# Kernel tuning notes

Hardware: AMD Instinct MI355X
Metric: run time of the kernel (lower is better)

Reference implementation:

```python
import jax, jax.numpy as jnp
import numpy as np
from jax import lax

B, H, W_IN, C = 32, 32, 32, 128   # NHWC input
KH, KW = 3, 3                     # kernel size (padding 'same', stride 1)
F = 512                           # filters


def setup_inputs() -> dict:
    key = jax.random.key(0)
    ks = jax.random.split(key, 10)
    # sparse factor shapes: (KH*KW*C, 1152), (1152, F), (F, F)
    d0, d1, d2, d3 = KH * KW * C, 1152, F, F
    x = jax.random.normal(ks[0], (B, H, W_IN, C), dtype=jnp.float32)
    k0 = jax.random.normal(ks[1], (d0, d1), dtype=jnp.float32) * (1.0 / np.sqrt(d0))
    k1 = jax.random.normal(ks[2], (d1, d2), dtype=jnp.float32) * (1.0 / np.sqrt(d1))
    k2 = jax.random.normal(ks[3], (d2, d3), dtype=jnp.float32) * (1.0 / np.sqrt(d2))
    # fixed binary sparsity masks (K.constant in the original build)
    m0 = jax.random.bernoulli(ks[4], 0.1, (d0, d1)).astype(jnp.float32)
    m1 = jax.random.bernoulli(ks[5], 0.1, (d1, d2)).astype(jnp.float32)
    m2 = jax.random.bernoulli(ks[6], 0.1, (d2, d3)).astype(jnp.float32)
    scale = jax.random.normal(ks[7], (1,), dtype=jnp.float32)
    bias = jax.random.normal(ks[8], (F,), dtype=jnp.float32) * 0.01
    return {"x": x, "k0": k0, "k1": k1, "k2": k2,
            "m0": m0, "m1": m1, "m2": m2, "scale": scale, "bias": bias}


def reference(x, k0, k1, k2, m0, m1, m2, scale, bias):
    # Chained masked sparse factors collapse (associativity) to one effective
    # filter matrix of shape (KH*KW*C, F); the im2col row flatten order in the
    # original is (h, w, c), which matches an HWIO reshape exactly.
    w_eff = (k0 * m0) @ (k1 * m1) @ (k2 * m2)          # (KH*KW*C, F)
    w = (w_eff * scale[0]).reshape(KH, KW, C, F)        # fold scalar scale into kernel
    out = lax.conv_general_dilated(
        x, w, window_strides=(1, 1), padding='SAME',
        dimension_numbers=('NHWC', 'HWIO', 'NHWC'))     # (B, H, W, F)
    return out + bias
```

## Files before the change

### kernel.cpp

```cpp
#include <hip/hip_runtime.h>

typedef __attribute__((ext_vector_type(8))) short short8;
typedef __attribute__((ext_vector_type(4))) float f32x4;

typedef __attribute__((address_space(1))) const unsigned gas_u32;
typedef __attribute__((address_space(3))) unsigned las_u32;

static __device__ __forceinline__ void g2l16(const void* g, void* l) {
  __builtin_amdgcn_global_load_lds((gas_u32*)g, (las_u32*)l, 16, 0, 0);
}

static __device__ __forceinline__ short f2bf(float f) {
  union { float f; unsigned u; } v; v.f = f;
  unsigned r = (v.u + 0x7FFFu + ((v.u >> 16) & 1u)) >> 16;
  return (short)r;
}

__global__ __launch_bounds__(256) void k_prep(const float* __restrict__ x,
                                              const float* __restrict__ k0f,
                                              const float* __restrict__ m0f,
                                              const float* __restrict__ scf,
                                              const float* __restrict__ k1f,
                                              const float* __restrict__ m1f,
                                              const float* __restrict__ k2f,
                                              const float* __restrict__ m2f,
                                              short* __restrict__ xbp,
                                              short* __restrict__ w1b,
                                              short* __restrict__ w2T,
                                              short* __restrict__ w3T) {
  __shared__ float tile[32][33];
  const int bb = blockIdx.x, tid = threadIdx.x;
  if (bb < 648) {
    int i = bb * 256 + tid;
    float s = scf[0];
    const f32x4* kk = (const f32x4*)k0f + (size_t)i * 2;
    const f32x4* mm = (const f32x4*)m0f + (size_t)i * 2;
    f32x4 a0 = kk[0], a1 = kk[1], b0 = mm[0], b1 = mm[1];
    short8 o;
    o[0] = f2bf(a0[0] * b0[0] * s); o[1] = f2bf(a0[1] * b0[1] * s);
    o[2] = f2bf(a0[2] * b0[2] * s); o[3] = f2bf(a0[3] * b0[3] * s);
    o[4] = f2bf(a1[0] * b1[0] * s); o[5] = f2bf(a1[1] * b1[1] * s);
    o[6] = f2bf(a1[2] * b1[2] * s); o[7] = f2bf(a1[3] * b1[3] * s);
    ((short8*)w1b)[i] = o;
  } else if (bb < 1480) {
    const float *kf, *mf; short* outp; int D, F, idx;
    if (bb < 1224) { kf = k1f; mf = m1f; outp = w2T; D = 1152; F = 512; idx = bb - 648; }
    else           { kf = k2f; mf = m2f; outp = w3T; D = 512;  F = 512; idx = bb - 1224; }
    int f0 = (idx & 15) * 32, d0 = (idx >> 4) * 32;
    int tx = tid & 31, ty = tid >> 5;
#pragma unroll
    for (int i = 0; i < 4; ++i) {
      int d = d0 + ty + i * 8;
      size_t ix = (size_t)d * F + f0 + tx;
      tile[ty + i * 8][tx] = kf[ix] * mf[ix];
    }
    __syncthreads();
#pragma unroll
    for (int i = 0; i < 4; ++i) {
      int f = f0 + ty + i * 8;
      outp[(size_t)f * D + d0 + tx] = f2bf(tile[tx][ty + i * 8]);
    }
  } else {
    int i = (bb - 1480) * 256 + tid;
    int c8 = i & 15;
    int t = i >> 4;
    int wp = t % 34, t2 = t / 34;
    int hp = t2 % 34, b = t2 / 34;
    short8 o = {};
    if (hp >= 1 && hp <= 32 && wp >= 1 && wp <= 32) {
      const f32x4* s = (const f32x4*)(x + (((size_t)((b << 5) + hp - 1) << 5) + (wp - 1)) * 128 + c8 * 8);
      f32x4 a = s[0], bb2 = s[1];
      o[0] = f2bf(a[0]); o[1] = f2bf(a[1]); o[2] = f2bf(a[2]); o[3] = f2bf(a[3]);
      o[4] = f2bf(bb2[0]); o[5] = f2bf(bb2[1]); o[6] = f2bf(bb2[2]); o[7] = f2bf(bb2[3]);
    }
    ((short8*)xbp)[i] = o;
  }
}

__global__ __launch_bounds__(256) void k_gemm64(const short* __restrict__ A,
                                                const short* __restrict__ BT,
                                                short* __restrict__ C, int M, int N, int K) {
  __shared__ __align__(16) short As[64][64];
  __shared__ __align__(16) short Bs[64][64];
  const int ntiles = N >> 6;
  const int m0 = (blockIdx.x / ntiles) << 6, n0 = (blockIdx.x % ntiles) << 6;
  const int tid = threadIdx.x;
  const int lane = tid & 63, wv = tid >> 6;
  const int wr = (wv >> 1) * 32, wc = (wv & 1) * 32;
  const int lr = lane & 15, lk = (lane >> 4) * 8;

  f32x4 acc[2][2] = {};

  const int rr = tid >> 3, c8 = (tid & 7) * 8;
  unsigned abase[2], bbase[2];
#pragma unroll
  for (int j = 0; j < 2; ++j) {
    abase[j] = (unsigned)(m0 + j * 32 + rr) * K + c8;
    bbase[j] = (unsigned)(n0 + j * 32 + rr) * K + c8;
  }
  short* AsL = &As[0][0];
  short* BsL = &Bs[0][0];
  const int lo = wv * 512;

  for (int kt = 0; kt < K; kt += 64) {
#pragma unroll
    for (int j = 0; j < 2; ++j) g2l16(A + abase[j] + kt, AsL + j * 2048 + lo);
#pragma unroll
    for (int j = 0; j < 2; ++j) g2l16(BT + bbase[j] + kt, BsL + j * 2048 + lo);
    __syncthreads();
#pragma unroll
    for (int ks = 0; ks < 2; ++ks) {
      const int ko = ks * 32 + lk;
      short8 af[2], bf[2];
#pragma unroll
      for (int i = 0; i < 2; ++i) af[i] = *(const short8*)&As[wr + i * 16 + lr][ko];
#pragma unroll
      for (int i = 0; i < 2; ++i) bf[i] = *(const short8*)&Bs[wc + i * 16 + lr][ko];
#pragma unroll
      for (int mi = 0; mi < 2; ++mi)
#pragma unroll
        for (int ni = 0; ni < 2; ++ni)
          acc[mi][ni] = __builtin_amdgcn_mfma_f32_16x16x32_bf16(af[mi], bf[ni], acc[mi][ni], 0, 0, 0);
    }
    __syncthreads();
  }
#pragma unroll
  for (int mi = 0; mi < 2; ++mi) {
    const int row = m0 + wr + mi * 16 + (lane >> 4) * 4;
#pragma unroll
    for (int ni = 0; ni < 2; ++ni) {
      const int col = n0 + wc + ni * 16 + lr;
#pragma unroll
      for (int q = 0; q < 4; ++q)
        C[(size_t)(row + q) * N + col] = f2bf(acc[mi][ni][q]);
    }
  }
}

#define MF(a_, b_, c_) __builtin_amdgcn_mfma_f32_16x16x32_bf16(a_, b_, c_, 0, 0, 0)

#define RD_A(mf_, ks_) \
  (*(const short8*)&As[wr * 128 + (mf_) * 16 + lr][(((ks_) * 4 + lh) ^ (lr & 7)) * 8])
#define RD_B(nf_, ks_) \
  (*(const short8*)&Bs[wc * 32 + (nf_) * 16 + lr][(((ks_) * 4 + lh) ^ (lr & 7)) * 8])

#define LOADB do { \
  bfr[0][0] = RD_B(0, 0); bfr[0][1] = RD_B(0, 1); \
  bfr[1][0] = RD_B(1, 0); bfr[1][1] = RD_B(1, 1); } while (0)

#define STAGE_AQ(q_, tt_) do { \
  const int tc_ = (tt_) > 17 ? 17 : (tt_); \
  const int khw_ = tc_ >> 1; const int kh_ = (khw_ * 11) >> 5; const int kw_ = khw_ - kh_ * 3; \
  const int ao_ = (kh_ * 34 + kw_) * 128 + ((tc_ & 1) << 6) + (q_) * 4352; \
  g2l16(xbp + aBase + ao_, &As[aRow + (q_) * 32][0]); } while (0)

#define STAGE_BH(j_, tt_) do { \
  const int tc_ = (tt_) > 17 ? 17 : (tt_); \
  g2l16(wT + bBase + (j_) * 73728 + tc_ * 64, &Bs[(j_) * 64 + bRow][0]); } while (0)

#define MFMA8(p_) \
  acc[2*(p_)  ][0] = MF(a0k0, bfr[0][0], acc[2*(p_)  ][0]); \
  acc[2*(p_)  ][1] = MF(a0k0, bfr[1][0], acc[2*(p_)  ][1]); \
  acc[2*(p_)+1][0] = MF(a1k0, bfr[0][0], acc[2*(p_)+1][0]); \
  acc[2*(p_)+1][1] = MF(a1k0, bfr[1][0], acc[2*(p_)+1][1]); \
  acc[2*(p_)  ][0] = MF(a0k1, bfr[0][1], acc[2*(p_)  ][0]); \
  acc[2*(p_)  ][1] = MF(a0k1, bfr[1][1], acc[2*(p_)  ][1]); \
  acc[2*(p_)+1][0] = MF(a1k1, bfr[0][1], acc[2*(p_)+1][0]); \
  acc[2*(p_)+1][1] = MF(a1k1, bfr[1][1], acc[2*(p_)+1][1]);

#define PHASE(p_, PRE, WAITV, ...) do { \
  PRE; \
  short8 a0k0 = RD_A(2*(p_), 0),   a0k1 = RD_A(2*(p_), 1); \
  short8 a1k0 = RD_A(2*(p_)+1, 0), a1k1 = RD_A(2*(p_)+1, 1); \
  __builtin_amdgcn_s_barrier(); \
  asm volatile("s_waitcnt lgkmcnt(0)" ::: "memory"); \
  __builtin_amdgcn_sched_barrier(0); \
  __VA_ARGS__ \
  __builtin_amdgcn_s_setprio(1); \
  MFMA8(p_) \
  __builtin_amdgcn_s_setprio(0); \
  WAITV; \
  __builtin_amdgcn_s_barrier(); \
} while (0)

#define VM5 asm volatile("s_waitcnt vmcnt(5)" ::: "memory")
#define VM3 asm volatile("s_waitcnt vmcnt(3)" ::: "memory")

__global__ __launch_bounds__(512, 4) void k_conv(const short* __restrict__ xbp,
                                                 const short* __restrict__ wT,
                                                 const float* __restrict__ bias,
                                                 float* __restrict__ out) {
  __shared__ __align__(16) short As[256][64];
  __shared__ __align__(16) short Bs[128][64];
  int bid = blockIdx.x;
  bid = (bid & 7) * 64 + (bid >> 3);
  const int mt = bid >> 2, nt = bid & 3;
  const int m0 = mt << 8, n0 = nt << 7;
  const int tid = threadIdx.x;
  const int lane = tid & 63, wid = tid >> 6;
  const int wr = wid >> 2, wc = wid & 3;
  const int lr = lane & 15, lh = lane >> 4;

  f32x4 acc[8][2] = {};
  short8 bfr[2][2];

  const int wrB = (wid >> 2) * 128;
  const int rsub = (wid & 3) * 8 + (lane >> 3);
  const int sw = (lane & 7) ^ (lane >> 3);
  const int aRow = wrB + (wid & 3) * 8;
  const int bRow = wid * 8;

  const int Mb = m0 + wrB + rsub;
  const int b = Mb >> 10, h0 = (Mb >> 5) & 31, w = Mb & 31;
  const unsigned aBase = (unsigned)((b * 34 + h0) * 34 + w) * 128 + sw * 8;
  const unsigned bBase = (unsigned)(n0 + wid * 8 + (lane >> 3)) * 1152 + sw * 8;

  STAGE_BH(0, 0); STAGE_BH(1, 0);
  STAGE_AQ(0, 0); STAGE_AQ(1, 0); STAGE_AQ(2, 0); STAGE_AQ(3, 0);
  asm volatile("s_waitcnt vmcnt(0)" ::: "memory");
  __builtin_amdgcn_s_barrier();

  for (int t = 0; t < 18; ++t) {
    const int tn = t + 1;
    PHASE(0, LOADB, VM5, STAGE_BH(0, tn); STAGE_BH(1, tn); STAGE_AQ(0, tn););
    PHASE(1, ,      VM5, STAGE_AQ(1, tn););
    PHASE(2, ,      VM5, STAGE_AQ(2, tn););
    PHASE(3, ,      VM3, STAGE_AQ(3, tn););
  }
  asm volatile("s_waitcnt vmcnt(0)" ::: "memory");

  const int orow = m0 + wr * 128, ocol = n0 + wc * 32;
#pragma unroll
  for (int mf = 0; mf < 8; ++mf) {
    const int row = orow + mf * 16 + lh * 4;
#pragma unroll
    for (int nf = 0; nf < 2; ++nf) {
      const int col = ocol + nf * 16 + lr;
      const float bv = bias[col];
#pragma unroll
      for (int q = 0; q < 4; ++q)
        out[(size_t)(row + q) * 512 + col] = acc[mf][nf][q] + bv;
    }
  }
}

extern "C" void kernel_launch(void* const* d_in, const int* in_sizes, int n_in,
                              void* d_out, int out_size, void* d_ws, size_t ws_size,
                              hipStream_t stream) {
  (void)in_sizes; (void)n_in; (void)out_size; (void)ws_size;
  const float* x    = (const float*)d_in[0];
  const float* k0   = (const float*)d_in[1];
  const float* k1   = (const float*)d_in[2];
  const float* k2   = (const float*)d_in[3];
  const float* m0   = (const float*)d_in[4];
  const float* m1   = (const float*)d_in[5];
  const float* m2   = (const float*)d_in[6];
  const float* sc   = (const float*)d_in[7];
  const float* bias = (const float*)d_in[8];
  float* out = (float*)d_out;
  char* ws = (char*)d_ws;

  short* xbp = (short*)(ws);
  short* w1b = (short*)(ws + 9469952);
  short* w2T = (short*)(ws + 12124160);
  short* w3T = (short*)(ws + 13303808);
  short* A1b = (short*)(ws + 13828096);
  short* wET = (short*)(ws + 15007744);

  k_prep<<<3792, 256, 0, stream>>>(x, k0, m0, sc, k1, m1, k2, m2, xbp, w1b, w2T, w3T);
  k_gemm64<<<144, 256, 0, stream>>>(w1b, w2T, A1b, 1152, 512, 1152);
  k_gemm64<<<144, 256, 0, stream>>>(w3T, A1b, wET, 512, 1152, 512);
  k_conv<<<512, 512, 0, stream>>>(xbp, wET, bias, out);
}
```

Baseline: 76.17 us.

## Retile conv to 128x128 with 256 threads and hide input conversion in GEMM launches

The conv kernel moves from 256x128 tiles with 512 threads to 128x128 tiles with 256 threads and 1024 blocks. Each wave now computes a 64x64 sub-tile with a 4x4 accumulator set, and each K step runs in two phases instead of four. The padded bf16 input conversion is split out of the prep kernel and spread across extra blocks of the two small weight-GEMM launches, filling CUs those 144-block GEMMs leave idle. The trade-off is less data reuse per tile and more blocks, in exchange for better occupancy and a shorter prep kernel.

```diff
diff --git a/kernel.cpp b/kernel.cpp
--- a/kernel.cpp
+++ b/kernel.cpp
@@ -16,18 +16,32 @@
   return (short)r;
 }
 
-__global__ __launch_bounds__(256) void k_prep(const float* __restrict__ x,
-                                              const float* __restrict__ k0f,
-                                              const float* __restrict__ m0f,
-                                              const float* __restrict__ scf,
-                                              const float* __restrict__ k1f,
-                                              const float* __restrict__ m1f,
-                                              const float* __restrict__ k2f,
-                                              const float* __restrict__ m2f,
-                                              short* __restrict__ xbp,
-                                              short* __restrict__ w1b,
-                                              short* __restrict__ w2T,
-                                              short* __restrict__ w3T) {
+static __device__ __forceinline__ void xcvt_body(const float* __restrict__ x,
+                                                 short* __restrict__ xbp, int i) {
+  int c8 = i & 15;
+  int t = i >> 4;
+  int wp = t % 34, t2 = t / 34;
+  int hp = t2 % 34, b = t2 / 34;
+  short8 o = {};
+  if (hp >= 1 && hp <= 32 && wp >= 1 && wp <= 32) {
+    const f32x4* s = (const f32x4*)(x + (((size_t)((b << 5) + hp - 1) << 5) + (wp - 1)) * 128 + c8 * 8);
+    f32x4 a = s[0], bb2 = s[1];
+    o[0] = f2bf(a[0]); o[1] = f2bf(a[1]); o[2] = f2bf(a[2]); o[3] = f2bf(a[3]);
+    o[4] = f2bf(bb2[0]); o[5] = f2bf(bb2[1]); o[6] = f2bf(bb2[2]); o[7] = f2bf(bb2[3]);
+  }
+  ((short8*)xbp)[i] = o;
+}
+
+__global__ __launch_bounds__(256) void k_prepw(const float* __restrict__ k0f,
+                                               const float* __restrict__ m0f,
+                                               const float* __restrict__ scf,
+                                               const float* __restrict__ k1f,
+                                               const float* __restrict__ m1f,
+                                               const float* __restrict__ k2f,
+                                               const float* __restrict__ m2f,
+                                               short* __restrict__ w1b,
+                                               short* __restrict__ w2T,
+                                               short* __restrict__ w3T) {
   __shared__ float tile[32][33];
   const int bb = blockIdx.x, tid = threadIdx.x;
   if (bb < 648) {
@@ -42,7 +56,7 @@
     o[4] = f2bf(a1[0] * b1[0] * s); o[5] = f2bf(a1[1] * b1[1] * s);
     o[6] = f2bf(a1[2] * b1[2] * s); o[7] = f2bf(a1[3] * b1[3] * s);
     ((short8*)w1b)[i] = o;
-  } else if (bb < 1480) {
+  } else {
     const float *kf, *mf; short* outp; int D, F, idx;
     if (bb < 1224) { kf = k1f; mf = m1f; outp = w2T; D = 1152; F = 512; idx = bb - 648; }
     else           { kf = k2f; mf = m2f; outp = w3T; D = 512;  F = 512; idx = bb - 1224; }
@@ -60,28 +74,20 @@
       int f = f0 + ty + i * 8;
       outp[(size_t)f * D + d0 + tx] = f2bf(tile[tx][ty + i * 8]);
     }
-  } else {
-    int i = (bb - 1480) * 256 + tid;
-    int c8 = i & 15;
-    int t = i >> 4;
-    int wp = t % 34, t2 = t / 34;
-    int hp = t2 % 34, b = t2 / 34;
-    short8 o = {};
-    if (hp >= 1 && hp <= 32 && wp >= 1 && wp <= 32) {
-      const f32x4* s = (const f32x4*)(x + (((size_t)((b << 5) + hp - 1) << 5) + (wp - 1)) * 128 + c8 * 8);
-      f32x4 a = s[0], bb2 = s[1];
-      o[0] = f2bf(a[0]); o[1] = f2bf(a[1]); o[2] = f2bf(a[2]); o[3] = f2bf(a[3]);
-      o[4] = f2bf(bb2[0]); o[5] = f2bf(bb2[1]); o[6] = f2bf(bb2[2]); o[7] = f2bf(bb2[3]);
-    }
-    ((short8*)xbp)[i] = o;
-  }
-}
-
-__global__ __launch_bounds__(256) void k_gemm64(const short* __restrict__ A,
-                                                const short* __restrict__ BT,
-                                                short* __restrict__ C, int M, int N, int K) {
+  }
+}
+
+__global__ __launch_bounds__(256) void k_gemm64x(const short* __restrict__ A,
+                                                 const short* __restrict__ BT,
+                                                 short* __restrict__ C, int M, int N, int K,
+                                                 const float* __restrict__ x,
+                                                 short* __restrict__ xbp, int xoff) {
   __shared__ __align__(16) short As[64][64];
   __shared__ __align__(16) short Bs[64][64];
+  if (blockIdx.x >= 144) {
+    xcvt_body(x, xbp, (xoff + (int)blockIdx.x - 144) * 256 + (int)threadIdx.x);
+    return;
+  }
   const int ntiles = N >> 6;
   const int m0 = (blockIdx.x / ntiles) << 6, n0 = (blockIdx.x % ntiles) << 6;
   const int tid = threadIdx.x;
@@ -140,101 +146,116 @@
 #define MF(a_, b_, c_) __builtin_amdgcn_mfma_f32_16x16x32_bf16(a_, b_, c_, 0, 0, 0)
 
 #define RD_A(mf_, ks_) \
-  (*(const short8*)&As[wr * 128 + (mf_) * 16 + lr][(((ks_) * 4 + lh) ^ (lr & 7)) * 8])
+  (*(const short8*)&As[wr * 64 + (mf_) * 16 + lr][(((ks_) * 4 + lh) ^ (lr & 7)) * 8])
 #define RD_B(nf_, ks_) \
-  (*(const short8*)&Bs[wc * 32 + (nf_) * 16 + lr][(((ks_) * 4 + lh) ^ (lr & 7)) * 8])
+  (*(const short8*)&Bs[wc * 64 + (nf_) * 16 + lr][(((ks_) * 4 + lh) ^ (lr & 7)) * 8])
 
 #define LOADB do { \
   bfr[0][0] = RD_B(0, 0); bfr[0][1] = RD_B(0, 1); \
-  bfr[1][0] = RD_B(1, 0); bfr[1][1] = RD_B(1, 1); } while (0)
+  bfr[1][0] = RD_B(1, 0); bfr[1][1] = RD_B(1, 1); \
+  bfr[2][0] = RD_B(2, 0); bfr[2][1] = RD_B(2, 1); \
+  bfr[3][0] = RD_B(3, 0); bfr[3][1] = RD_B(3, 1); } while (0)
 
 #define STAGE_AQ(q_, tt_) do { \
   const int tc_ = (tt_) > 17 ? 17 : (tt_); \
   const int khw_ = tc_ >> 1; const int kh_ = (khw_ * 11) >> 5; const int kw_ = khw_ - kh_ * 3; \
   const int ao_ = (kh_ * 34 + kw_) * 128 + ((tc_ & 1) << 6) + (q_) * 4352; \
-  g2l16(xbp + aBase + ao_, &As[aRow + (q_) * 32][0]); } while (0)
-
-#define STAGE_BH(j_, tt_) do { \
+  g2l16(xbp + aBase + ao_, &As[(q_) * 32 + wid * 8][0]); } while (0)
+
+#define STAGE_BQ(j_, tt_) do { \
   const int tc_ = (tt_) > 17 ? 17 : (tt_); \
-  g2l16(wT + bBase + (j_) * 73728 + tc_ * 64, &Bs[(j_) * 64 + bRow][0]); } while (0)
-
-#define MFMA8(p_) \
-  acc[2*(p_)  ][0] = MF(a0k0, bfr[0][0], acc[2*(p_)  ][0]); \
-  acc[2*(p_)  ][1] = MF(a0k0, bfr[1][0], acc[2*(p_)  ][1]); \
-  acc[2*(p_)+1][0] = MF(a1k0, bfr[0][0], acc[2*(p_)+1][0]); \
-  acc[2*(p_)+1][1] = MF(a1k0, bfr[1][0], acc[2*(p_)+1][1]); \
-  acc[2*(p_)  ][0] = MF(a0k1, bfr[0][1], acc[2*(p_)  ][0]); \
-  acc[2*(p_)  ][1] = MF(a0k1, bfr[1][1], acc[2*(p_)  ][1]); \
-  acc[2*(p_)+1][0] = MF(a1k1, bfr[0][1], acc[2*(p_)+1][0]); \
-  acc[2*(p_)+1][1] = MF(a1k1, bfr[1][1], acc[2*(p_)+1][1]);
-
-#define PHASE(p_, PRE, WAITV, ...) do { \
-  PRE; \
-  short8 a0k0 = RD_A(2*(p_), 0),   a0k1 = RD_A(2*(p_), 1); \
-  short8 a1k0 = RD_A(2*(p_)+1, 0), a1k1 = RD_A(2*(p_)+1, 1); \
-  __builtin_amdgcn_s_barrier(); \
-  asm volatile("s_waitcnt lgkmcnt(0)" ::: "memory"); \
-  __builtin_amdgcn_sched_barrier(0); \
-  __VA_ARGS__ \
-  __builtin_amdgcn_s_setprio(1); \
-  MFMA8(p_) \
-  __builtin_amdgcn_s_setprio(0); \
-  WAITV; \
-  __builtin_amdgcn_s_barrier(); \
-} while (0)
-
-#define VM5 asm volatile("s_waitcnt vmcnt(5)" ::: "memory")
-#define VM3 asm volatile("s_waitcnt vmcnt(3)" ::: "memory")
-
-__global__ __launch_bounds__(512, 4) void k_conv(const short* __restrict__ xbp,
+  g2l16(wT + bBase + (j_) * 36864 + tc_ * 64, &Bs[(j_) * 32 + wid * 8][0]); } while (0)
+
+#define MFMA16(mb_) \
+  acc[mb_  ][0] = MF(a0k0, bfr[0][0], acc[mb_  ][0]); \
+  acc[mb_  ][1] = MF(a0k0, bfr[1][0], acc[mb_  ][1]); \
+  acc[mb_  ][2] = MF(a0k0, bfr[2][0], acc[mb_  ][2]); \
+  acc[mb_  ][3] = MF(a0k0, bfr[3][0], acc[mb_  ][3]); \
+  acc[mb_+1][0] = MF(a1k0, bfr[0][0], acc[mb_+1][0]); \
+  acc[mb_+1][1] = MF(a1k0, bfr[1][0], acc[mb_+1][1]); \
+  acc[mb_+1][2] = MF(a1k0, bfr[2][0], acc[mb_+1][2]); \
+  acc[mb_+1][3] = MF(a1k0, bfr[3][0], acc[mb_+1][3]); \
+  acc[mb_  ][0] = MF(a0k1, bfr[0][1], acc[mb_  ][0]); \
+  acc[mb_  ][1] = MF(a0k1, bfr[1][1], acc[mb_  ][1]); \
+  acc[mb_  ][2] = MF(a0k1, bfr[2][1], acc[mb_  ][2]); \
+  acc[mb_  ][3] = MF(a0k1, bfr[3][1], acc[mb_  ][3]); \
+  acc[mb_+1][0] = MF(a1k1, bfr[0][1], acc[mb_+1][0]); \
+  acc[mb_+1][1] = MF(a1k1, bfr[1][1], acc[mb_+1][1]); \
+  acc[mb_+1][2] = MF(a1k1, bfr[2][1], acc[mb_+1][2]); \
+  acc[mb_+1][3] = MF(a1k1, bfr[3][1], acc[mb_+1][3]);
+
+#define VM6 asm volatile("s_waitcnt vmcnt(6)" ::: "memory")
+#define VM2 asm volatile("s_waitcnt vmcnt(2)" ::: "memory")
+
+__global__ __launch_bounds__(256, 4) void k_conv(const short* __restrict__ xbp,
                                                  const short* __restrict__ wT,
                                                  const float* __restrict__ bias,
                                                  float* __restrict__ out) {
-  __shared__ __align__(16) short As[256][64];
+  __shared__ __align__(16) short As[128][64];
   __shared__ __align__(16) short Bs[128][64];
   int bid = blockIdx.x;
-  bid = (bid & 7) * 64 + (bid >> 3);
+  bid = (bid & 7) * 128 + (bid >> 3);
   const int mt = bid >> 2, nt = bid & 3;
-  const int m0 = mt << 8, n0 = nt << 7;
+  const int m0 = mt << 7, n0 = nt << 7;
   const int tid = threadIdx.x;
   const int lane = tid & 63, wid = tid >> 6;
-  const int wr = wid >> 2, wc = wid & 3;
+  const int wr = wid >> 1, wc = wid & 1;
   const int lr = lane & 15, lh = lane >> 4;
 
-  f32x4 acc[8][2] = {};
-  short8 bfr[2][2];
-
-  const int wrB = (wid >> 2) * 128;
-  const int rsub = (wid & 3) * 8 + (lane >> 3);
-  const int sw = (lane & 7) ^ (lane >> 3);
-  const int aRow = wrB + (wid & 3) * 8;
-  const int bRow = wid * 8;
-
-  const int Mb = m0 + wrB + rsub;
+  f32x4 acc[4][4] = {};
+  short8 bfr[4][2];
+
+  const int r = tid >> 3;
+  const int sw = (tid & 7) ^ (r & 7);
+  const int Mb = m0 + r;
   const int b = Mb >> 10, h0 = (Mb >> 5) & 31, w = Mb & 31;
   const unsigned aBase = (unsigned)((b * 34 + h0) * 34 + w) * 128 + sw * 8;
-  const unsigned bBase = (unsigned)(n0 + wid * 8 + (lane >> 3)) * 1152 + sw * 8;
-
-  STAGE_BH(0, 0); STAGE_BH(1, 0);
+  const unsigned bBase = (unsigned)(n0 + r) * 1152 + sw * 8;
+
   STAGE_AQ(0, 0); STAGE_AQ(1, 0); STAGE_AQ(2, 0); STAGE_AQ(3, 0);
+  STAGE_BQ(0, 0); STAGE_BQ(1, 0); STAGE_BQ(2, 0); STAGE_BQ(3, 0);
   asm volatile("s_waitcnt vmcnt(0)" ::: "memory");
   __builtin_amdgcn_s_barrier();
 
   for (int t = 0; t < 18; ++t) {
     const int tn = t + 1;
-    PHASE(0, LOADB, VM5, STAGE_BH(0, tn); STAGE_BH(1, tn); STAGE_AQ(0, tn););
-    PHASE(1, ,      VM5, STAGE_AQ(1, tn););
-    PHASE(2, ,      VM5, STAGE_AQ(2, tn););
-    PHASE(3, ,      VM3, STAGE_AQ(3, tn););
+    {
+      LOADB;
+      short8 a0k0 = RD_A(0, 0), a0k1 = RD_A(0, 1);
+      short8 a1k0 = RD_A(1, 0), a1k1 = RD_A(1, 1);
+      __builtin_amdgcn_s_barrier();
+      asm volatile("s_waitcnt lgkmcnt(0)" ::: "memory");
+      __builtin_amdgcn_sched_barrier(0);
+      STAGE_AQ(0, tn); STAGE_AQ(2, tn);
+      STAGE_BQ(0, tn); STAGE_BQ(1, tn); STAGE_BQ(2, tn); STAGE_BQ(3, tn);
+      __builtin_amdgcn_s_setprio(1);
+      MFMA16(0)
+      __builtin_amdgcn_s_setprio(0);
+      VM6;
+      __builtin_amdgcn_s_barrier();
+    }
+    {
+      short8 a0k0 = RD_A(2, 0), a0k1 = RD_A(2, 1);
+      short8 a1k0 = RD_A(3, 0), a1k1 = RD_A(3, 1);
+      __builtin_amdgcn_s_barrier();
+      asm volatile("s_waitcnt lgkmcnt(0)" ::: "memory");
+      __builtin_amdgcn_sched_barrier(0);
+      STAGE_AQ(1, tn); STAGE_AQ(3, tn);
+      __builtin_amdgcn_s_setprio(1);
+      MFMA16(2)
+      __builtin_amdgcn_s_setprio(0);
+      VM2;
+      __builtin_amdgcn_s_barrier();
+    }
   }
   asm volatile("s_waitcnt vmcnt(0)" ::: "memory");
 
-  const int orow = m0 + wr * 128, ocol = n0 + wc * 32;
-#pragma unroll
-  for (int mf = 0; mf < 8; ++mf) {
+  const int orow = m0 + wr * 64, ocol = n0 + wc * 64;
+#pragma unroll
+  for (int mf = 0; mf < 4; ++mf) {
     const int row = orow + mf * 16 + lh * 4;
 #pragma unroll
-    for (int nf = 0; nf < 2; ++nf) {
+    for (int nf = 0; nf < 4; ++nf) {
       const int col = ocol + nf * 16 + lr;
       const float bv = bias[col];
 #pragma unroll
@@ -267,8 +288,8 @@
   short* A1b = (short*)(ws + 13828096);
   short* wET = (short*)(ws + 15007744);
 
-  k_prep<<<3792, 256, 0, stream>>>(x, k0, m0, sc, k1, m1, k2, m2, xbp, w1b, w2T, w3T);
-  k_gemm64<<<144, 256, 0, stream>>>(w1b, w2T, A1b, 1152, 512, 1152);
-  k_gemm64<<<144, 256, 0, stream>>>(w3T, A1b, wET, 512, 1152, 512);
-  k_conv<<<512, 512, 0, stream>>>(xbp, wET, bias, out);
-}
+  k_prepw<<<1480, 256, 0, stream>>>(k0, m0, sc, k1, m1, k2, m2, w1b, w2T, w3T);
+  k_gemm64x<<<1300, 256, 0, stream>>>(w1b, w2T, A1b, 1152, 512, 1152, x, xbp, 0);
+  k_gemm64x<<<1300, 256, 0, stream>>>(w3T, A1b, wET, 512, 1152, 512, x, xbp, 1156);
+  k_conv<<<1024, 256, 0, stream>>>(xbp, wET, bias, out);
+}
```

New measurement: 87.47 us. 1.15x slower.
